# Kernel tuning notes

Measured on AMD Instinct MI355X. Metric: run time of the kernel, lower is better.

Reference implementation:

```python
import jax, jax.numpy as jnp
import numpy as np

C_M, C_Z, H, C_HID = 256, 128, 8, 32
N_SEQ, N_RES = 64, 384
INF = 1e9
EPS = 1e-5


def layernorm(x, w, b):
    mu = jnp.mean(x, axis=-1, keepdims=True)
    var = jnp.mean(jnp.square(x - mu), axis=-1, keepdims=True)
    return (x - mu) * jax.lax.rsqrt(var + EPS) * w + b


def setup_inputs() -> dict:
    key = jax.random.key(0)
    ks = jax.random.split(key, 6)
    m = jax.random.normal(ks[0], (N_SEQ, N_RES, C_M), dtype=jnp.float32)
    z = jax.random.normal(ks[1], (N_RES, N_RES, C_Z), dtype=jnp.float32)
    mask = jnp.ones((N_SEQ, N_RES), dtype=jnp.float32)
    return {
        "m": m,
        "z": z,
        "mask": mask,
        "ln_m_w": jnp.ones((C_M,), jnp.float32),
        "ln_m_b": jnp.zeros((C_M,), jnp.float32),
        "ln_z_w": jnp.ones((C_Z,), jnp.float32),
        "ln_z_b": jnp.zeros((C_Z,), jnp.float32),
        "W_z": jax.random.normal(ks[2], (C_Z, H), jnp.float32) * 0.05,
        "W_v": jax.random.normal(ks[3], (C_M, H * C_HID), jnp.float32) * 0.05,
        "W_g": jax.random.normal(ks[4], (C_M, H * C_HID), jnp.float32) * 0.05,
        "W_o": jax.random.normal(ks[5], (H * C_HID, C_M), jnp.float32) * 0.05,
    }


def reference(m, z, mask, ln_m_w, ln_m_b, ln_z_w, ln_z_b, W_z, W_v, W_g, W_o):
    S, N = m.shape[0], m.shape[1]
    # mask: max over MSA rows, keepdim -> [1, N]; bias -> [1,1,1,N]
    mask_max = jnp.max(mask, axis=-2, keepdims=True)
    mask_bias = (INF * (mask_max - 1.0))[:, None, None, :]  # [1,1,1,N]
    # pair bias: LN(z) @ W_z -> [N,N,H] -> [H,N,N]
    zb = layernorm(z, ln_z_w, ln_z_b) @ W_z  # [N,N,H]
    zb = jnp.transpose(zb, (2, 0, 1))  # [H,N,N]
    # LN on m
    m_ln = layernorm(m, ln_m_w, ln_m_b)  # [S,N,C_m]
    # values: [S,N,H*c] -> [S,H,N,c]
    v = (m_ln @ W_v).reshape(S, N, H, C_HID).transpose(0, 2, 1, 3)
    # attention weights from summed biases (no QK): [1,H,N,N] after broadcast
    a = jax.nn.softmax(mask_bias + zb[None], axis=-1)  # [1,H,N,N]
    # o = a @ v  -> [S,H,N,c]
    o = jnp.einsum('hqk,shkc->shqc', a[0], v)
    o = o.transpose(0, 2, 1, 3)  # [S,N,H,c]
    # sigmoid gate
    g = jax.nn.sigmoid(m_ln @ W_g).reshape(S, N, H, C_HID)
    o = (o * g).reshape(S, N, H * C_HID)
    return o @ W_o  # [S,N,C_m]
```

## Files before the change

kernel.cpp:

```cpp
#include <hip/hip_runtime.h>
#include <math.h>

#define S 64
#define NRES 384
#define CM 256
#define CZ 128
#define NH 8
#define CH 32
#define HC 256

typedef unsigned short u16;
typedef __attribute__((ext_vector_type(8))) short bf16x8;
typedef __attribute__((ext_vector_type(4))) float f32x4;
typedef __attribute__((ext_vector_type(8))) unsigned short ushort8;
typedef __attribute__((ext_vector_type(4))) unsigned short ushort4_t;

#define OFF_BIAS 0
#define OFF_WT   200704
#define OFF_WOT  462848
#define OFF_A    593920
#define OFF_VT   2953216
#define OFF_G    15536128
#define OFF_O    28119040
#define OFF_MLN  40701952
#define OFF_ZB   OFF_O
#define OFF_WWT  OFF_VT
#define OFF_C1   (OFF_VT + 4096)
#define OFF_C2   (OFF_VT + 4160)

__device__ __forceinline__ u16 f2bf(float f) {
    union { float f; unsigned int u; } v; v.f = f;
    unsigned int u = v.u;
    u += 0x7fff + ((u >> 16) & 1);
    return (u16)(u >> 16);
}
__device__ __forceinline__ float bf2f(u16 b) {
    union { float f; unsigned int u; } v; v.u = ((unsigned int)b) << 16;
    return v.f;
}

__global__ __launch_bounds__(256) void k_prep_all(
        const float* __restrict__ mask, const float* __restrict__ Wz,
        const float* __restrict__ lzw, const float* __restrict__ lzb,
        const float* __restrict__ Wv, const float* __restrict__ Wg,
        const float* __restrict__ Wo, const float* __restrict__ m,
        const float* __restrict__ lmw, const float* __restrict__ lmb,
        float* __restrict__ bias, u16* __restrict__ WWT,
        float* __restrict__ C1, float* __restrict__ C2,
        u16* __restrict__ Wt, u16* __restrict__ Wot,
        u16* __restrict__ mln) {
    const int bid = blockIdx.x, tid = threadIdx.x;
    if (bid < 2) {
        const int k = bid * 256 + tid;
        if (k < NRES) {
            float mx = -1e30f;
            for (int s = 0; s < S; ++s) mx = fmaxf(mx, mask[s * NRES + k]);
            bias[k] = 1e9f * (mx - 1.0f);
        }
    } else if (bid == 2) {
        __shared__ float sW[CZ][NH], sB[CZ][NH];
        const int c = tid;
        if (c < CZ) {
            #pragma unroll
            for (int h = 0; h < NH; ++h) {
                const float wz = Wz[c * NH + h];
                const float ww = lzw[c] * wz;
                sW[c][h] = ww;
                sB[c][h] = lzb[c] * wz;
                WWT[h * CZ + c] = f2bf(ww);
                WWT[(NH + h) * CZ + c] = 0;
            }
        }
        __syncthreads();
        if (c < NH) {
            float s1 = 0.f, s2 = 0.f;
            for (int k = 0; k < CZ; ++k) { s1 += sW[k][c]; s2 += sB[k][c]; }
            C1[c] = s1; C2[c] = s2;
        } else if (c < 16) {
            C1[c] = 0.f; C2[c] = 0.f;
        }
    } else if (bid < 515) {
        const int i = (bid - 3) * 256 + tid;
        const int n = i >> 8, k = i & 255;
        const float v = (n < HC) ? Wv[(size_t)k * HC + n] : Wg[(size_t)k * HC + (n - HC)];
        Wt[i] = f2bf(v);
    } else if (bid < 771) {
        const int i = (bid - 515) * 256 + tid;
        const int n = i >> 8, k = i & 255;
        Wot[i] = f2bf(Wo[(size_t)k * CM + n]);
    } else {
        const int row = (bid - 771) * 4 + (tid >> 6);
        const int lane = tid & 63;
        const float4 x = *(const float4*)&m[(size_t)row * CM + lane * 4];
        float sm = x.x + x.y + x.z + x.w;
        float sq = x.x*x.x + x.y*x.y + x.z*x.z + x.w*x.w;
        #pragma unroll
        for (int off = 32; off >= 1; off >>= 1) {
            sm += __shfl_xor(sm, off);
            sq += __shfl_xor(sq, off);
        }
        const float mu = sm * (1.0f / CM);
        const float var = sq * (1.0f / CM) - mu * mu;
        const float rs = rsqrtf(var + 1e-5f);
        const float4 w4 = *(const float4*)&lmw[lane * 4];
        const float4 b4 = *(const float4*)&lmb[lane * 4];
        u16 t4[4];
        t4[0] = f2bf((x.x - mu) * rs * w4.x + b4.x);
        t4[1] = f2bf((x.y - mu) * rs * w4.y + b4.y);
        t4[2] = f2bf((x.z - mu) * rs * w4.z + b4.z);
        t4[3] = f2bf((x.w - mu) * rs * w4.w + b4.w);
        *(ushort4_t*)&mln[(size_t)row * CM + lane * 4] = *(ushort4_t*)t4;
    }
}

__global__ __launch_bounds__(256) void k_zb(const float* __restrict__ z,
        const u16* __restrict__ WWT, const float* __restrict__ C1,
        const float* __restrict__ C2, float* __restrict__ zb) {
    __shared__ float sMu[4][16], sRs[4][16];
    const int tid = threadIdx.x, wave = tid >> 6, lane = tid & 63;
    const int rl = lane & 15, kg = lane >> 4;
    const int row0 = blockIdx.x * 64 + wave * 16;
    const float* zrow = z + (size_t)(row0 + rl) * CZ + kg * 8;
    bf16x8 af[4];
    float sm = 0.f, sq = 0.f;
    #pragma unroll
    for (int t = 0; t < 4; ++t) {
        const float4 x0 = *(const float4*)&zrow[t * 32];
        const float4 x1 = *(const float4*)&zrow[t * 32 + 4];
        float xs[8] = {x0.x, x0.y, x0.z, x0.w, x1.x, x1.y, x1.z, x1.w};
        u16 tmp[8];
        #pragma unroll
        for (int e = 0; e < 8; ++e) {
            sm += xs[e]; sq += xs[e] * xs[e];
            tmp[e] = f2bf(xs[e]);
        }
        af[t] = *(bf16x8*)tmp;
    }
    sm += __shfl_xor(sm, 16); sq += __shfl_xor(sq, 16);
    sm += __shfl_xor(sm, 32); sq += __shfl_xor(sq, 32);
    const float mu = sm * (1.0f / CZ);
    const float var = sq * (1.0f / CZ) - mu * mu;
    const float rs = rsqrtf(var + 1e-5f);
    if (lane < 16) { sMu[wave][lane] = mu; sRs[wave][lane] = rs; }
    const u16* wbase = WWT + rl * CZ + kg * 8;
    bf16x8 bfr[4];
    #pragma unroll
    for (int t = 0; t < 4; ++t) bfr[t] = *(const bf16x8*)&wbase[t * 32];
    f32x4 acc = {};
    #pragma unroll
    for (int t = 0; t < 4; ++t)
        acc = __builtin_amdgcn_mfma_f32_16x16x32_bf16(af[t], bfr[t], acc, 0, 0, 0);
    __syncthreads();
    const float c1 = C1[rl], c2 = C2[rl];
    #pragma unroll
    for (int r = 0; r < 4; ++r) {
        const int rr = kg * 4 + r;
        const float p = sRs[wave][rr] * (acc[r] - sMu[wave][rr] * c1) + c2;
        if (rl < 8) zb[(size_t)(row0 + rr) * NH + rl] = p;
    }
}

__global__ __launch_bounds__(256) void k_soft(const float* __restrict__ zb,
        const float* __restrict__ bias, u16* __restrict__ a_out) {
    const int w = blockIdx.x * 4 + (threadIdx.x >> 6);
    const int lane = threadIdx.x & 63;
    const int h = w & 7, q = w >> 3;
    float v[6];
    float mx = -1e30f;
    #pragma unroll
    for (int t = 0; t < 6; ++t) {
        const int k = lane + 64 * t;
        v[t] = zb[((size_t)q * NRES + k) * NH + h] + bias[k];
        mx = fmaxf(mx, v[t]);
    }
    #pragma unroll
    for (int off = 32; off >= 1; off >>= 1) mx = fmaxf(mx, __shfl_xor(mx, off));
    float sum = 0.f;
    #pragma unroll
    for (int t = 0; t < 6; ++t) { v[t] = expf(v[t] - mx); sum += v[t]; }
    #pragma unroll
    for (int off = 32; off >= 1; off >>= 1) sum += __shfl_xor(sum, off);
    const float inv = 1.0f / sum;
    #pragma unroll
    for (int t = 0; t < 6; ++t)
        a_out[((size_t)h * NRES + q) * NRES + lane + 64 * t] = f2bf(v[t] * inv);
}

__global__ __launch_bounds__(256) void k_gemm_vg(const u16* __restrict__ mln,
        const u16* __restrict__ Wt, u16* __restrict__ vt, u16* __restrict__ g_) {
    __shared__ u16 As[128][40];
    __shared__ u16 Bs[128][40];
    const int tid = threadIdx.x;
    const int xcd = blockIdx.x & 7, idx = blockIdx.x >> 3;
    const int nt = idx & 3, mt = xcd * 24 + (idx >> 2);
    const int m0 = mt * 128, n0 = nt * 128;
    const int wave = tid >> 6, lane = tid & 63;
    const int wm = (wave >> 1) * 64, wn = (wave & 1) * 64;
    const int rl = lane & 15, kg = lane >> 4;
    const int sr = tid >> 1, sh = (tid & 1) * 16;
    const u16* arow = mln + (size_t)(m0 + sr) * CM;
    const u16* wrow = Wt + (size_t)(n0 + sr) * CM;
    const bool vhalf = (n0 < HC);
    f32x4 acc[4][4] = {};
    for (int kt = 0; kt < CM; kt += 32) {
        if (kt) __syncthreads();
        *(ushort8*)&As[sr][sh]     = *(const ushort8*)&arow[kt + sh];
        *(ushort8*)&As[sr][sh + 8] = *(const ushort8*)&arow[kt + sh + 8];
        *(ushort8*)&Bs[sr][sh]     = *(const ushort8*)&wrow[kt + sh];
        *(ushort8*)&Bs[sr][sh + 8] = *(const ushort8*)&wrow[kt + sh + 8];
        __syncthreads();
        bf16x8 af[4], bfr[4];
        #pragma unroll
        for (int i = 0; i < 4; ++i) af[i]  = *(const bf16x8*)&As[wm + i*16 + rl][kg*8];
        #pragma unroll
        for (int j = 0; j < 4; ++j) bfr[j] = *(const bf16x8*)&Bs[wn + j*16 + rl][kg*8];
        if (vhalf) {
            #pragma unroll
            for (int j = 0; j < 4; ++j)
                #pragma unroll
                for (int i = 0; i < 4; ++i)
                    acc[j][i] = __builtin_amdgcn_mfma_f32_16x16x32_bf16(bfr[j], af[i], acc[j][i], 0, 0, 0);
        } else {
            #pragma unroll
            for (int i = 0; i < 4; ++i)
                #pragma unroll
                for (int j = 0; j < 4; ++j)
                    acc[i][j] = __builtin_amdgcn_mfma_f32_16x16x32_bf16(af[i], bfr[j], acc[i][j], 0, 0, 0);
        }
    }
    if (vhalf) {
        #pragma unroll
        for (int j = 0; j < 4; ++j)
            #pragma unroll
            for (int r = 0; r < 4; ++r) {
                const int vcol = n0 + wn + j*16 + kg*4 + r;
                const int h = vcol >> 5, c = vcol & 31;
                #pragma unroll
                for (int i = 0; i < 4; ++i) {
                    const int mrowb = m0 + wm + i*16;
                    const int s = mrowb / NRES;
                    const int nn = mrowb - s * NRES + rl;
                    vt[(((size_t)h * S + s) * CH + c) * NRES + nn] = f2bf(acc[j][i][r]);
                }
            }
    } else {
        #pragma unroll
        for (int i = 0; i < 4; ++i)
            #pragma unroll
            for (int r = 0; r < 4; ++r) {
                const int row = m0 + wm + i*16 + kg*4 + r;
                #pragma unroll
                for (int j = 0; j < 4; ++j) {
                    const int gc = n0 + wn + j*16 + rl - HC;
                    g_[(size_t)row * HC + gc] = f2bf(1.0f / (1.0f + expf(-acc[i][j][r])));
                }
            }
    }
}

__global__ __launch_bounds__(256) void k_attn2(const u16* __restrict__ a_,
        const u16* __restrict__ vt, u16* __restrict__ o_) {
    __shared__ u16 As[128][40];
    __shared__ u16 Bs[128][40];
    const int tid = threadIdx.x;
    const int h = blockIdx.x & 7, rem = blockIdx.x >> 3;
    const int mt = rem >> 4, nt = rem & 15;
    const int q0 = mt * 128, sc0 = nt * 128;
    const int wave = tid >> 6, lane = tid & 63;
    const int wm = (wave >> 1) * 64, wn = (wave & 1) * 64;
    const int rl = lane & 15, kg = lane >> 4;
    const int sr = tid >> 1, sh = (tid & 1) * 16;
    const u16* arow = a_ + (size_t)h * NRES * NRES + (size_t)(q0 + sr) * NRES;
    const u16* vrow = vt + (size_t)h * S * CH * NRES + (size_t)(sc0 + sr) * NRES;
    f32x4 acc[4][4] = {};
    for (int kt = 0; kt < NRES; kt += 32) {
        if (kt) __syncthreads();
        *(ushort8*)&As[sr][sh]     = *(const ushort8*)&arow[kt + sh];
        *(ushort8*)&As[sr][sh + 8] = *(const ushort8*)&arow[kt + sh + 8];
        *(ushort8*)&Bs[sr][sh]     = *(const ushort8*)&vrow[kt + sh];
        *(ushort8*)&Bs[sr][sh + 8] = *(const ushort8*)&vrow[kt + sh + 8];
        __syncthreads();
        bf16x8 af[4], bfr[4];
        #pragma unroll
        for (int i = 0; i < 4; ++i) af[i]  = *(const bf16x8*)&As[wm + i*16 + rl][kg*8];
        #pragma unroll
        for (int j = 0; j < 4; ++j) bfr[j] = *(const bf16x8*)&Bs[wn + j*16 + rl][kg*8];
        #pragma unroll
        for (int i = 0; i < 4; ++i)
            #pragma unroll
            for (int j = 0; j < 4; ++j)
                acc[i][j] = __builtin_amdgcn_mfma_f32_16x16x32_bf16(af[i], bfr[j], acc[i][j], 0, 0, 0);
    }
    #pragma unroll
    for (int i = 0; i < 4; ++i)
        #pragma unroll
        for (int r = 0; r < 4; ++r) {
            const int q = q0 + wm + i*16 + kg*4 + r;
            #pragma unroll
            for (int j = 0; j < 4; ++j) {
                const int sc = sc0 + wn + j*16 + rl;
                const int s = sc >> 5, c = sc & 31;
                o_[(((size_t)s * NRES + q) * NH + h) * CH + c] = f2bf(acc[i][j][r]);
            }
        }
}

__global__ __launch_bounds__(256) void k_gemm_out(const u16* __restrict__ o_,
        const u16* __restrict__ g_, const u16* __restrict__ Wot,
        float* __restrict__ out) {
    __shared__ u16 As[128][40];
    __shared__ u16 Bs[128][40];
    const int tid = threadIdx.x;
    const int xcd = blockIdx.x & 7, idx = blockIdx.x >> 3;
    const int nt = idx & 1, mt = xcd * 24 + (idx >> 1);
    const int m0 = mt * 128, n0 = nt * 128;
    const int wave = tid >> 6, lane = tid & 63;
    const int wm = (wave >> 1) * 64, wn = (wave & 1) * 64;
    const int rl = lane & 15, kg = lane >> 4;
    const int sr = tid >> 1, sh = (tid & 1) * 16;
    const u16* orow = o_ + (size_t)(m0 + sr) * HC;
    const u16* grow = g_ + (size_t)(m0 + sr) * HC;
    const u16* wrow = Wot + (size_t)(n0 + sr) * HC;
    f32x4 acc[4][4] = {};
    for (int kt = 0; kt < HC; kt += 32) {
        if (kt) __syncthreads();
        {
            u16 tmp[16];
            const ushort8 ov0 = *(const ushort8*)&orow[kt + sh];
            const ushort8 ov1 = *(const ushort8*)&orow[kt + sh + 8];
            const ushort8 gv0 = *(const ushort8*)&grow[kt + sh];
            const ushort8 gv1 = *(const ushort8*)&grow[kt + sh + 8];
            #pragma unroll
            for (int p = 0; p < 8; ++p) {
                tmp[p]     = f2bf(bf2f(ov0[p]) * bf2f(gv0[p]));
                tmp[p + 8] = f2bf(bf2f(ov1[p]) * bf2f(gv1[p]));
            }
            *(ushort8*)&As[sr][sh]     = *(ushort8*)&tmp[0];
            *(ushort8*)&As[sr][sh + 8] = *(ushort8*)&tmp[8];
            *(ushort8*)&Bs[sr][sh]     = *(const ushort8*)&wrow[kt + sh];
            *(ushort8*)&Bs[sr][sh + 8] = *(const ushort8*)&wrow[kt + sh + 8];
        }
        __syncthreads();
        bf16x8 af[4], bfr[4];
        #pragma unroll
        for (int i = 0; i < 4; ++i) af[i]  = *(const bf16x8*)&As[wm + i*16 + rl][kg*8];
        #pragma unroll
        for (int j = 0; j < 4; ++j) bfr[j] = *(const bf16x8*)&Bs[wn + j*16 + rl][kg*8];
        #pragma unroll
        for (int i = 0; i < 4; ++i)
            #pragma unroll
            for (int j = 0; j < 4; ++j)
                acc[i][j] = __builtin_amdgcn_mfma_f32_16x16x32_bf16(af[i], bfr[j], acc[i][j], 0, 0, 0);
    }
    #pragma unroll
    for (int i = 0; i < 4; ++i)
        #pragma unroll
        for (int r = 0; r < 4; ++r) {
            const int row = m0 + wm + i*16 + kg*4 + r;
            #pragma unroll
            for (int j = 0; j < 4; ++j)
                out[(size_t)row * CM + n0 + wn + j*16 + rl] = acc[i][j][r];
        }
}

extern "C" void kernel_launch(void* const* d_in, const int* in_sizes, int n_in,
                              void* d_out, int out_size, void* d_ws, size_t ws_size,
                              hipStream_t stream) {
    const float* m      = (const float*)d_in[0];
    const float* z      = (const float*)d_in[1];
    const float* mask   = (const float*)d_in[2];
    const float* ln_m_w = (const float*)d_in[3];
    const float* ln_m_b = (const float*)d_in[4];
    const float* ln_z_w = (const float*)d_in[5];
    const float* ln_z_b = (const float*)d_in[6];
    const float* Wz     = (const float*)d_in[7];
    const float* Wv     = (const float*)d_in[8];
    const float* Wg     = (const float*)d_in[9];
    const float* Wo     = (const float*)d_in[10];
    float* out = (float*)d_out;
    char* ws = (char*)d_ws;

    float* bias = (float*)(ws + OFF_BIAS);
    u16* Wt     = (u16*)(ws + OFF_WT);
    u16* Wot    = (u16*)(ws + OFF_WOT);
    u16* a      = (u16*)(ws + OFF_A);
    u16* vtw    = (u16*)(ws + OFF_VT);
    u16* gw     = (u16*)(ws + OFF_G);
    u16* ow     = (u16*)(ws + OFF_O);
    u16* mlnw   = (u16*)(ws + OFF_MLN);
    float* zbw  = (float*)(ws + OFF_ZB);
    u16* WWT    = (u16*)(ws + OFF_WWT);
    float* C1   = (float*)(ws + OFF_C1);
    float* C2   = (float*)(ws + OFF_C2);

    k_prep_all<<<6915, 256, 0, stream>>>(mask, Wz, ln_z_w, ln_z_b, Wv, Wg, Wo, m,
                                         ln_m_w, ln_m_b, bias, WWT, C1, C2, Wt, Wot, mlnw);
    k_zb<<<2304, 256, 0, stream>>>(z, WWT, C1, C2, zbw);
    k_soft<<<768, 256, 0, stream>>>(zbw, bias, a);
    k_gemm_vg<<<192 * 4, 256, 0, stream>>>(mlnw, Wt, vtw, gw);
    k_attn2<<<384, 256, 0, stream>>>(a, vtw, ow);
    k_gemm_out<<<192 * 2, 256, 0, stream>>>(ow, gw, Wot, out);
}
```

Before: 90.30 us.

## Merge prep/zb and softmax/vg-gemm launches; stage GEMM tiles via global_load_lds

Folds the z pair-bias projection into the prep kernel. Each wave now recomputes the folded LN weights and column sums itself instead of reading them from a separate prep step. The softmax is merged into the V/G GEMM launch as extra blocks, cutting the kernel count from six to four. GEMM tile loads in the vg, attention and output kernels now use direct global-to-LDS loads into unpadded 32-wide LDS rows, which may add bank conflicts on the fragment reads in exchange for skipping the register round-trip.

```diff
diff --git a/kernel.cpp b/kernel.cpp
--- a/kernel.cpp
+++ b/kernel.cpp
@@ -24,9 +24,6 @@
 #define OFF_O    28119040
 #define OFF_MLN  40701952
 #define OFF_ZB   OFF_O
-#define OFF_WWT  OFF_VT
-#define OFF_C1   (OFF_VT + 4096)
-#define OFF_C2   (OFF_VT + 4160)
 
 __device__ __forceinline__ u16 f2bf(float f) {
     union { float f; unsigned int u; } v; v.f = f;
@@ -38,58 +35,102 @@
     union { float f; unsigned int u; } v; v.u = ((unsigned int)b) << 16;
     return v.f;
 }
-
-__global__ __launch_bounds__(256) void k_prep_all(
-        const float* __restrict__ mask, const float* __restrict__ Wz,
+__device__ __forceinline__ void gload16(const u16* g, u16* l) {
+    __builtin_amdgcn_global_load_lds(
+        (const __attribute__((address_space(1))) void*)g,
+        (__attribute__((address_space(3))) void*)l, 16, 0, 0);
+}
+
+__global__ __launch_bounds__(256) void k_stage1(
+        const float* __restrict__ z, const float* __restrict__ Wz,
         const float* __restrict__ lzw, const float* __restrict__ lzb,
+        const float* __restrict__ mask,
         const float* __restrict__ Wv, const float* __restrict__ Wg,
         const float* __restrict__ Wo, const float* __restrict__ m,
         const float* __restrict__ lmw, const float* __restrict__ lmb,
-        float* __restrict__ bias, u16* __restrict__ WWT,
-        float* __restrict__ C1, float* __restrict__ C2,
-        u16* __restrict__ Wt, u16* __restrict__ Wot,
-        u16* __restrict__ mln) {
+        float* __restrict__ zb, float* __restrict__ bias,
+        u16* __restrict__ Wt, u16* __restrict__ Wot, u16* __restrict__ mln) {
     const int bid = blockIdx.x, tid = threadIdx.x;
-    if (bid < 2) {
-        const int k = bid * 256 + tid;
+    if (bid < 2304) {
+        const int wave = tid >> 6, lane = tid & 63;
+        const int rl = lane & 15, kg = lane >> 4;
+        const int row0 = bid * 64 + wave * 16;
+        const float* zrow = z + (size_t)(row0 + rl) * CZ + kg * 8;
+        bf16x8 af[4];
+        float sm = 0.f, sq = 0.f;
+        #pragma unroll
+        for (int t = 0; t < 4; ++t) {
+            const float4 x0 = *(const float4*)&zrow[t * 32];
+            const float4 x1 = *(const float4*)&zrow[t * 32 + 4];
+            float xs[8] = {x0.x, x0.y, x0.z, x0.w, x1.x, x1.y, x1.z, x1.w};
+            u16 tmp[8];
+            #pragma unroll
+            for (int e = 0; e < 8; ++e) {
+                sm += xs[e]; sq += xs[e] * xs[e];
+                tmp[e] = f2bf(xs[e]);
+            }
+            af[t] = *(bf16x8*)tmp;
+        }
+        sm += __shfl_xor(sm, 16); sq += __shfl_xor(sq, 16);
+        sm += __shfl_xor(sm, 32); sq += __shfl_xor(sq, 32);
+        const float mu = sm * (1.0f / CZ);
+        const float var = sq * (1.0f / CZ) - mu * mu;
+        const float rs = rsqrtf(var + 1e-5f);
+        const int hh = lane & 7, seg = lane >> 3;
+        float s1 = 0.f, s2 = 0.f;
+        #pragma unroll
+        for (int ci = 0; ci < 16; ++ci) {
+            const int c = seg * 16 + ci;
+            const float wz = Wz[c * NH + hh];
+            s1 += lzw[c] * wz;
+            s2 += lzb[c] * wz;
+        }
+        #pragma unroll
+        for (int off = 8; off < 64; off <<= 1) {
+            s1 += __shfl_xor(s1, off);
+            s2 += __shfl_xor(s2, off);
+        }
+        bf16x8 bfr[4];
+        #pragma unroll
+        for (int t = 0; t < 4; ++t) {
+            u16 tmp[8];
+            #pragma unroll
+            for (int e = 0; e < 8; ++e) {
+                const int c = t * 32 + kg * 8 + e;
+                tmp[e] = (rl < 8) ? f2bf(lzw[c] * Wz[c * NH + rl]) : (u16)0;
+            }
+            bfr[t] = *(bf16x8*)tmp;
+        }
+        f32x4 acc = {};
+        #pragma unroll
+        for (int t = 0; t < 4; ++t)
+            acc = __builtin_amdgcn_mfma_f32_16x16x32_bf16(af[t], bfr[t], acc, 0, 0, 0);
+        #pragma unroll
+        for (int r = 0; r < 4; ++r) {
+            const int rr = kg * 4 + r;
+            const float mu_r = __shfl(mu, rr);
+            const float rs_r = __shfl(rs, rr);
+            const float p = rs_r * (acc[r] - mu_r * s1) + s2;
+            if (rl < 8) zb[(size_t)(row0 + rr) * NH + rl] = p;
+        }
+    } else if (bid < 2306) {
+        const int k = (bid - 2304) * 256 + tid;
         if (k < NRES) {
             float mx = -1e30f;
             for (int s = 0; s < S; ++s) mx = fmaxf(mx, mask[s * NRES + k]);
             bias[k] = 1e9f * (mx - 1.0f);
         }
-    } else if (bid == 2) {
-        __shared__ float sW[CZ][NH], sB[CZ][NH];
-        const int c = tid;
-        if (c < CZ) {
-            #pragma unroll
-            for (int h = 0; h < NH; ++h) {
-                const float wz = Wz[c * NH + h];
-                const float ww = lzw[c] * wz;
-                sW[c][h] = ww;
-                sB[c][h] = lzb[c] * wz;
-                WWT[h * CZ + c] = f2bf(ww);
-                WWT[(NH + h) * CZ + c] = 0;
-            }
-        }
-        __syncthreads();
-        if (c < NH) {
-            float s1 = 0.f, s2 = 0.f;
-            for (int k = 0; k < CZ; ++k) { s1 += sW[k][c]; s2 += sB[k][c]; }
-            C1[c] = s1; C2[c] = s2;
-        } else if (c < 16) {
-            C1[c] = 0.f; C2[c] = 0.f;
-        }
-    } else if (bid < 515) {
-        const int i = (bid - 3) * 256 + tid;
+    } else if (bid < 2818) {
+        const int i = (bid - 2306) * 256 + tid;
         const int n = i >> 8, k = i & 255;
         const float v = (n < HC) ? Wv[(size_t)k * HC + n] : Wg[(size_t)k * HC + (n - HC)];
         Wt[i] = f2bf(v);
-    } else if (bid < 771) {
-        const int i = (bid - 515) * 256 + tid;
+    } else if (bid < 3074) {
+        const int i = (bid - 2818) * 256 + tid;
         const int n = i >> 8, k = i & 255;
         Wot[i] = f2bf(Wo[(size_t)k * CM + n]);
     } else {
-        const int row = (bid - 771) * 4 + (tid >> 6);
+        const int row = (bid - 3074) * 4 + (tid >> 6);
         const int lane = tid & 63;
         const float4 x = *(const float4*)&m[(size_t)row * CM + lane * 4];
         float sm = x.x + x.y + x.z + x.w;
@@ -113,101 +154,60 @@
     }
 }
 
-__global__ __launch_bounds__(256) void k_zb(const float* __restrict__ z,
-        const u16* __restrict__ WWT, const float* __restrict__ C1,
-        const float* __restrict__ C2, float* __restrict__ zb) {
-    __shared__ float sMu[4][16], sRs[4][16];
-    const int tid = threadIdx.x, wave = tid >> 6, lane = tid & 63;
-    const int rl = lane & 15, kg = lane >> 4;
-    const int row0 = blockIdx.x * 64 + wave * 16;
-    const float* zrow = z + (size_t)(row0 + rl) * CZ + kg * 8;
-    bf16x8 af[4];
-    float sm = 0.f, sq = 0.f;
-    #pragma unroll
-    for (int t = 0; t < 4; ++t) {
-        const float4 x0 = *(const float4*)&zrow[t * 32];
-        const float4 x1 = *(const float4*)&zrow[t * 32 + 4];
-        float xs[8] = {x0.x, x0.y, x0.z, x0.w, x1.x, x1.y, x1.z, x1.w};
-        u16 tmp[8];
-        #pragma unroll
-        for (int e = 0; e < 8; ++e) {
-            sm += xs[e]; sq += xs[e] * xs[e];
-            tmp[e] = f2bf(xs[e]);
-        }
-        af[t] = *(bf16x8*)tmp;
-    }
-    sm += __shfl_xor(sm, 16); sq += __shfl_xor(sq, 16);
-    sm += __shfl_xor(sm, 32); sq += __shfl_xor(sq, 32);
-    const float mu = sm * (1.0f / CZ);
-    const float var = sq * (1.0f / CZ) - mu * mu;
-    const float rs = rsqrtf(var + 1e-5f);
-    if (lane < 16) { sMu[wave][lane] = mu; sRs[wave][lane] = rs; }
-    const u16* wbase = WWT + rl * CZ + kg * 8;
-    bf16x8 bfr[4];
-    #pragma unroll
-    for (int t = 0; t < 4; ++t) bfr[t] = *(const bf16x8*)&wbase[t * 32];
-    f32x4 acc = {};
-    #pragma unroll
-    for (int t = 0; t < 4; ++t)
-        acc = __builtin_amdgcn_mfma_f32_16x16x32_bf16(af[t], bfr[t], acc, 0, 0, 0);
-    __syncthreads();
-    const float c1 = C1[rl], c2 = C2[rl];
-    #pragma unroll
-    for (int r = 0; r < 4; ++r) {
-        const int rr = kg * 4 + r;
-        const float p = sRs[wave][rr] * (acc[r] - sMu[wave][rr] * c1) + c2;
-        if (rl < 8) zb[(size_t)(row0 + rr) * NH + rl] = p;
-    }
-}
-
-__global__ __launch_bounds__(256) void k_soft(const float* __restrict__ zb,
-        const float* __restrict__ bias, u16* __restrict__ a_out) {
-    const int w = blockIdx.x * 4 + (threadIdx.x >> 6);
-    const int lane = threadIdx.x & 63;
-    const int h = w & 7, q = w >> 3;
-    float v[6];
-    float mx = -1e30f;
-    #pragma unroll
-    for (int t = 0; t < 6; ++t) {
-        const int k = lane + 64 * t;
-        v[t] = zb[((size_t)q * NRES + k) * NH + h] + bias[k];
-        mx = fmaxf(mx, v[t]);
-    }
-    #pragma unroll
-    for (int off = 32; off >= 1; off >>= 1) mx = fmaxf(mx, __shfl_xor(mx, off));
-    float sum = 0.f;
-    #pragma unroll
-    for (int t = 0; t < 6; ++t) { v[t] = expf(v[t] - mx); sum += v[t]; }
-    #pragma unroll
-    for (int off = 32; off >= 1; off >>= 1) sum += __shfl_xor(sum, off);
-    const float inv = 1.0f / sum;
-    #pragma unroll
-    for (int t = 0; t < 6; ++t)
-        a_out[((size_t)h * NRES + q) * NRES + lane + 64 * t] = f2bf(v[t] * inv);
-}
-
-__global__ __launch_bounds__(256) void k_gemm_vg(const u16* __restrict__ mln,
-        const u16* __restrict__ Wt, u16* __restrict__ vt, u16* __restrict__ g_) {
-    __shared__ u16 As[128][40];
-    __shared__ u16 Bs[128][40];
-    const int tid = threadIdx.x;
-    const int xcd = blockIdx.x & 7, idx = blockIdx.x >> 3;
+__global__ __launch_bounds__(256) void k_stage2(
+        const u16* __restrict__ mln, const u16* __restrict__ Wt,
+        const float* __restrict__ zb, const float* __restrict__ bias,
+        u16* __restrict__ vt, u16* __restrict__ g_, u16* __restrict__ a_out) {
+    __shared__ u16 As[128][32];
+    __shared__ u16 Bs[128][32];
+    const int bid = blockIdx.x, tid = threadIdx.x;
+    if (bid >= 768) {
+        const int w = (bid - 768) * 4 + (tid >> 6);
+        const int lane = tid & 63;
+        const int h = w & 7, q = w >> 3;
+        float v[6];
+        float mx = -1e30f;
+        #pragma unroll
+        for (int t = 0; t < 6; ++t) {
+            const int k = lane + 64 * t;
+            v[t] = zb[((size_t)q * NRES + k) * NH + h] + bias[k];
+            mx = fmaxf(mx, v[t]);
+        }
+        #pragma unroll
+        for (int off = 32; off >= 1; off >>= 1) mx = fmaxf(mx, __shfl_xor(mx, off));
+        float sum = 0.f;
+        #pragma unroll
+        for (int t = 0; t < 6; ++t) { v[t] = expf(v[t] - mx); sum += v[t]; }
+        #pragma unroll
+        for (int off = 32; off >= 1; off >>= 1) sum += __shfl_xor(sum, off);
+        const float inv = 1.0f / sum;
+        #pragma unroll
+        for (int t = 0; t < 6; ++t)
+            a_out[((size_t)h * NRES + q) * NRES + lane + 64 * t] = f2bf(v[t] * inv);
+        return;
+    }
+    const int xcd = bid & 7, idx = bid >> 3;
     const int nt = idx & 3, mt = xcd * 24 + (idx >> 2);
     const int m0 = mt * 128, n0 = nt * 128;
     const int wave = tid >> 6, lane = tid & 63;
     const int wm = (wave >> 1) * 64, wn = (wave & 1) * 64;
     const int rl = lane & 15, kg = lane >> 4;
-    const int sr = tid >> 1, sh = (tid & 1) * 16;
-    const u16* arow = mln + (size_t)(m0 + sr) * CM;
-    const u16* wrow = Wt + (size_t)(n0 + sr) * CM;
+    const int lr = lane >> 2, lk = (lane & 3) * 8;
+    const int wr = wave * 32;
+    const u16* ag  = mln + (size_t)(m0 + wr + lr) * CM + lk;
+    const u16* ag2 = ag + 16 * CM;
+    const u16* bg  = Wt + (size_t)(n0 + wr + lr) * CM + lk;
+    const u16* bg2 = bg + 16 * CM;
+    u16* al  = &As[wr][0];
+    u16* al2 = &As[wr + 16][0];
+    u16* bl  = &Bs[wr][0];
+    u16* bl2 = &Bs[wr + 16][0];
     const bool vhalf = (n0 < HC);
     f32x4 acc[4][4] = {};
     for (int kt = 0; kt < CM; kt += 32) {
         if (kt) __syncthreads();
-        *(ushort8*)&As[sr][sh]     = *(const ushort8*)&arow[kt + sh];
-        *(ushort8*)&As[sr][sh + 8] = *(const ushort8*)&arow[kt + sh + 8];
-        *(ushort8*)&Bs[sr][sh]     = *(const ushort8*)&wrow[kt + sh];
-        *(ushort8*)&Bs[sr][sh + 8] = *(const ushort8*)&wrow[kt + sh + 8];
+        gload16(ag + kt, al);  gload16(ag2 + kt, al2);
+        gload16(bg + kt, bl);  gload16(bg2 + kt, bl2);
         __syncthreads();
         bf16x8 af[4], bfr[4];
         #pragma unroll
@@ -260,8 +260,8 @@
 
 __global__ __launch_bounds__(256) void k_attn2(const u16* __restrict__ a_,
         const u16* __restrict__ vt, u16* __restrict__ o_) {
-    __shared__ u16 As[128][40];
-    __shared__ u16 Bs[128][40];
+    __shared__ u16 As[128][32];
+    __shared__ u16 Bs[128][32];
     const int tid = threadIdx.x;
     const int h = blockIdx.x & 7, rem = blockIdx.x >> 3;
     const int mt = rem >> 4, nt = rem & 15;
@@ -269,16 +269,21 @@
     const int wave = tid >> 6, lane = tid & 63;
     const int wm = (wave >> 1) * 64, wn = (wave & 1) * 64;
     const int rl = lane & 15, kg = lane >> 4;
-    const int sr = tid >> 1, sh = (tid & 1) * 16;
-    const u16* arow = a_ + (size_t)h * NRES * NRES + (size_t)(q0 + sr) * NRES;
-    const u16* vrow = vt + (size_t)h * S * CH * NRES + (size_t)(sc0 + sr) * NRES;
+    const int lr = lane >> 2, lk = (lane & 3) * 8;
+    const int wr = wave * 32;
+    const u16* ag  = a_ + (size_t)h * NRES * NRES + (size_t)(q0 + wr + lr) * NRES + lk;
+    const u16* ag2 = ag + 16 * NRES;
+    const u16* bg  = vt + (size_t)h * S * CH * NRES + (size_t)(sc0 + wr + lr) * NRES + lk;
+    const u16* bg2 = bg + 16 * NRES;
+    u16* al  = &As[wr][0];
+    u16* al2 = &As[wr + 16][0];
+    u16* bl  = &Bs[wr][0];
+    u16* bl2 = &Bs[wr + 16][0];
     f32x4 acc[4][4] = {};
     for (int kt = 0; kt < NRES; kt += 32) {
         if (kt) __syncthreads();
-        *(ushort8*)&As[sr][sh]     = *(const ushort8*)&arow[kt + sh];
-        *(ushort8*)&As[sr][sh + 8] = *(const ushort8*)&arow[kt + sh + 8];
-        *(ushort8*)&Bs[sr][sh]     = *(const ushort8*)&vrow[kt + sh];
-        *(ushort8*)&Bs[sr][sh + 8] = *(const ushort8*)&vrow[kt + sh + 8];
+        gload16(ag + kt, al);  gload16(ag2 + kt, al2);
+        gload16(bg + kt, bl);  gload16(bg2 + kt, bl2);
         __syncthreads();
         bf16x8 af[4], bfr[4];
         #pragma unroll
@@ -309,7 +314,7 @@
         const u16* __restrict__ g_, const u16* __restrict__ Wot,
         float* __restrict__ out) {
     __shared__ u16 As[128][40];
-    __shared__ u16 Bs[128][40];
+    __shared__ u16 Bs[128][32];
     const int tid = threadIdx.x;
     const int xcd = blockIdx.x & 7, idx = blockIdx.x >> 3;
     const int nt = idx & 1, mt = xcd * 24 + (idx >> 1);
@@ -317,13 +322,19 @@
     const int wave = tid >> 6, lane = tid & 63;
     const int wm = (wave >> 1) * 64, wn = (wave & 1) * 64;
     const int rl = lane & 15, kg = lane >> 4;
+    const int lr = lane >> 2, lk = (lane & 3) * 8;
+    const int wr = wave * 32;
     const int sr = tid >> 1, sh = (tid & 1) * 16;
     const u16* orow = o_ + (size_t)(m0 + sr) * HC;
     const u16* grow = g_ + (size_t)(m0 + sr) * HC;
-    const u16* wrow = Wot + (size_t)(n0 + sr) * HC;
+    const u16* bg  = Wot + (size_t)(n0 + wr + lr) * HC + lk;
+    const u16* bg2 = bg + 16 * HC;
+    u16* bl  = &Bs[wr][0];
+    u16* bl2 = &Bs[wr + 16][0];
     f32x4 acc[4][4] = {};
     for (int kt = 0; kt < HC; kt += 32) {
         if (kt) __syncthreads();
+        gload16(bg + kt, bl);  gload16(bg2 + kt, bl2);
         {
             u16 tmp[16];
             const ushort8 ov0 = *(const ushort8*)&orow[kt + sh];
@@ -337,8 +348,6 @@
             }
             *(ushort8*)&As[sr][sh]     = *(ushort8*)&tmp[0];
             *(ushort8*)&As[sr][sh + 8] = *(ushort8*)&tmp[8];
-            *(ushort8*)&Bs[sr][sh]     = *(const ushort8*)&wrow[kt + sh];
-            *(ushort8*)&Bs[sr][sh + 8] = *(const ushort8*)&wrow[kt + sh + 8];
         }
         __syncthreads();
         bf16x8 af[4], bfr[4];
@@ -389,15 +398,10 @@
     u16* ow     = (u16*)(ws + OFF_O);
     u16* mlnw   = (u16*)(ws + OFF_MLN);
     float* zbw  = (float*)(ws + OFF_ZB);
-    u16* WWT    = (u16*)(ws + OFF_WWT);
-    float* C1   = (float*)(ws + OFF_C1);
-    float* C2   = (float*)(ws + OFF_C2);
-
-    k_prep_all<<<6915, 256, 0, stream>>>(mask, Wz, ln_z_w, ln_z_b, Wv, Wg, Wo, m,
-                                         ln_m_w, ln_m_b, bias, WWT, C1, C2, Wt, Wot, mlnw);
-    k_zb<<<2304, 256, 0, stream>>>(z, WWT, C1, C2, zbw);
-    k_soft<<<768, 256, 0, stream>>>(zbw, bias, a);
-    k_gemm_vg<<<192 * 4, 256, 0, stream>>>(mlnw, Wt, vtw, gw);
+
+    k_stage1<<<9218, 256, 0, stream>>>(z, Wz, ln_z_w, ln_z_b, mask, Wv, Wg, Wo,
+                                       m, ln_m_w, ln_m_b, zbw, bias, Wt, Wot, mlnw);
+    k_stage2<<<1536, 256, 0, stream>>>(mlnw, Wt, zbw, bias, vtw, gw, a);
     k_attn2<<<384, 256, 0, stream>>>(a, vtw, ow);
-    k_gemm_out<<<192 * 2, 256, 0, stream>>>(ow, gw, Wot, out);
-}
+    k_gemm_out<<<384, 256, 0, stream>>>(ow, gw, Wot, out);
+}
```

New measurement: 85.00 us. 5.9% less time.
